# Kernel optimization log

Measured on AMD Instinct MI355X. Metric: run time of the kernel, lower is better.

## Reference

```python
import jax, jax.numpy as jnp
import numpy as np

B, C, H, W = 8, 512, 64, 64
CI = C // 8  # inter_channels = 64


def setup_inputs() -> dict:
    key = jax.random.key(0)
    k = jax.random.split(key, 8)
    s = 0.02
    return {
        "x": jax.random.normal(k[0], (B, C, H, W), dtype=jnp.float32),
        "wq": jax.random.normal(k[1], (CI, C), dtype=jnp.float32) * s,
        "bq": jnp.zeros((CI,), dtype=jnp.float32),
        "wk": jax.random.normal(k[2], (CI, C), dtype=jnp.float32) * s,
        "bk": jnp.zeros((CI,), dtype=jnp.float32),
        "wv": jax.random.normal(k[3], (C, C), dtype=jnp.float32) * s,
        "bv": jnp.zeros((C,), dtype=jnp.float32),
        # original inits gamma to 0 (which kills attention branch); use a
        # nonzero value so the attention path contributes to output/grads
        "gamma": jax.random.normal(k[4], (1,), dtype=jnp.float32),
    }


def reference(x, wq, bq, wk, bk, wv, bv, gamma):
    b, c, h, w = x.shape
    n = h * w
    xf = x.reshape(b, c, n)  # (B, C, HW)
    # 1x1 convs == per-pixel linear layers
    q = jnp.einsum("oc,bcn->bon", wq, xf) + bq[None, :, None]  # (B, CI, HW)
    k_ = jnp.einsum("oc,bcn->bon", wk, xf) + bk[None, :, None]  # (B, CI, HW)
    v = jnp.einsum("oc,bcn->bon", wv, xf) + bv[None, :, None]  # (B, C, HW)
    # energy[b, i, j] = <q[:, i], k[:, j]>  -> softmax over j
    energy = jnp.einsum("bdn,bdm->bnm", q, k_)  # (B, HW, HW)
    attn = jax.nn.softmax(energy, axis=-1)
    # note: torch code does bmm(value, attention) -> out[:, c, j] = sum_i v[:, c, i] * attn[:, i, j]
    out = jnp.einsum("bci,bij->bcj", v, attn).reshape(b, c, h, w)
    return gamma[0] * out + x
```

## Files before the change

### kernel.cpp

```cpp
#include <hip/hip_runtime.h>
#include <hip/hip_bf16.h>

#define N_TOK 4096
#define CCH   512

using f32x4  = __attribute__((ext_vector_type(4))) float;
using f32x16 = __attribute__((ext_vector_type(16))) float;
using bf16x4 = __attribute__((ext_vector_type(4))) short;
using bf16x8 = __attribute__((ext_vector_type(8))) short;
using u32x4  = __attribute__((ext_vector_type(4))) unsigned int;

__device__ __forceinline__ short f2bf(float f) {
  __hip_bfloat16 h = __float2bfloat16(f);
  return __builtin_bit_cast(short, h);
}

__device__ __forceinline__ unsigned pkexp(float a, float b) {
  unsigned ua = __builtin_bit_cast(unsigned, __expf(a));
  unsigned ub = __builtin_bit_cast(unsigned, __expf(b));
  ua = ua + 0x7fffu + ((ua >> 16) & 1u);
  ub = ub + 0x7fffu + ((ub >> 16) & 1u);
  return (ua >> 16) | (ub & 0xffff0000u);
}

__device__ __forceinline__ f32x4 mfma16(bf16x8 a, bf16x8 b, f32x4 c) {
  return __builtin_amdgcn_mfma_f32_16x16x32_bf16(a, b, c, 0, 0, 0);
}
__device__ __forceinline__ f32x16 mfma32(bf16x8 a, bf16x8 b, f32x16 c) {
  return __builtin_amdgcn_mfma_f32_32x32x16_bf16(a, b, c, 0, 0, 0);
}

__device__ __forceinline__ void gload16(const void* g, void* l) {
  __builtin_amdgcn_global_load_lds(
      (const __attribute__((address_space(1))) void*)g,
      (__attribute__((address_space(3))) void*)l, 16, 0, 0);
}

__device__ __forceinline__ void stage_tile(short* lds, const short* src, int src_stride,
                                           int granules, int tid, int nthr) {
  for (int g = tid; g < granules; g += nthr) {
    int r = g >> 3, c16 = g & 7;
    bf16x8 v = *(const bf16x8*)(src + r * src_stride + c16 * 8);
    *(bf16x8*)(lds + r * 64 + ((c16 ^ (r & 7)) * 8)) = v;
  }
}

__device__ __forceinline__ bf16x8 read_frag(const short* lds, int row0, int ks, int lane) {
  int r = row0 + (lane & 15);
  int c16 = ks * 4 + (lane >> 4);
  return *(const bf16x8*)(lds + r * 64 + ((c16 ^ (r & 7)) * 8));
}

__global__ void k_conv_w(const float* wq, const float* wk, const float* wv,
                         const float* bq, const float* bk,
                         short* wqk_bf, short* wv_bf, float* bqk) {
  int idx = blockIdx.x * blockDim.x + threadIdx.x;
  int stride = gridDim.x * blockDim.x;
  const int n1 = 128 * 512;
  const int n2 = 512 * 512;
  for (int i = idx; i < n1; i += stride) {
    int d = i >> 9, c = i & 511;
    float v = (d < 64) ? wq[d * 512 + c] : wk[(d - 64) * 512 + c];
    wqk_bf[i] = f2bf(v);
  }
  for (int i = idx; i < n2; i += stride) wv_bf[i] = f2bf(wv[i]);
  if (idx < 128) bqk[idx] = (idx < 64) ? bq[idx] : bk[idx - 64];
}

__global__ __launch_bounds__(256) void k_transpose_x(const float* x, short* xT) {
  __shared__ float tile[64][65];
  int b = blockIdx.z, c0 = blockIdx.y * 64, n0 = blockIdx.x * 64;
  int tid = threadIdx.x;
  int col = tid & 63, rowb = tid >> 6;
  for (int r = rowb; r < 64; r += 4)
    tile[r][col] = x[((long)b * CCH + c0 + r) * N_TOK + n0 + col];
  __syncthreads();
  for (int r = rowb; r < 64; r += 4)
    xT[((long)b * N_TOK + n0 + r) * CCH + c0 + col] = f2bf(tile[col][r]);
}

__global__ __launch_bounds__(256) void k_gemm_nt(
    const short* A, long long Ab, const short* Bt, long long Bb,
    short* out, long long Ob, int out_stride,
    const float* bias, int bias_row, const float* colscale, long long cs_stride, int K) {
  __shared__ short Al[128 * 64], Bl[128 * 64];
  int b = blockIdx.z;
  int m0 = blockIdx.y * 128, n0 = blockIdx.x * 128;
  int tid = threadIdx.x, lane = tid & 63, w = tid >> 6;
  int wm = w >> 1, wn = w & 1;
  const short* Ap = A + b * Ab + (long long)m0 * K;
  const short* Bp = Bt + b * Bb + (long long)n0 * K;
  f32x4 acc[4][4] = {};
  for (int kt = 0; kt < K; kt += 64) {
    __syncthreads();
    stage_tile(Al, Ap + kt, K, 1024, tid, 256);
    stage_tile(Bl, Bp + kt, K, 1024, tid, 256);
    __syncthreads();
    for (int ks = 0; ks < 2; ++ks) {
      bf16x8 af[4], bfr[4];
      for (int i = 0; i < 4; ++i) af[i] = read_frag(Al, wm * 64 + i * 16, ks, lane);
      for (int i = 0; i < 4; ++i) bfr[i] = read_frag(Bl, wn * 64 + i * 16, ks, lane);
      for (int mf = 0; mf < 4; ++mf)
        for (int nf = 0; nf < 4; ++nf)
          acc[mf][nf] = mfma16(af[mf], bfr[nf], acc[mf][nf]);
    }
  }
  for (int mf = 0; mf < 4; ++mf)
    for (int nf = 0; nf < 4; ++nf)
      for (int t = 0; t < 4; ++t) {
        int m = m0 + wm * 64 + mf * 16 + (lane >> 4) * 4 + t;
        int n = n0 + wn * 64 + nf * 16 + (lane & 15);
        float v = acc[mf][nf][t];
        v += bias_row ? bias[m] : bias[n];
        if (colscale) v *= colscale[b * cs_stride + n];
        out[b * Ob + (long long)m * out_stride + n] = f2bf(v);
      }
}

__global__ __launch_bounds__(256) void k_passA(const short* __restrict__ qkT,
                                               float* __restrict__ Zinv) {
  __shared__ short ql[128 * 64];
  __shared__ short kl[2][128 * 64];
  __shared__ float zbuf[4][128];
  const int b = blockIdx.y, i0 = blockIdx.x * 128;
  const int tid = threadIdx.x, lane = tid & 63, w = tid >> 6;
  const int l31 = lane & 31, hi = lane >> 5;
  const int x7 = l31 & 7;

  stage_tile(ql, qkT + ((long long)b * N_TOK + i0) * 128, 128, 1024, tid, 256);

  const short* ksrc[4];
#pragma unroll
  for (int q = 0; q < 4; ++q) {
    int idx = (w * 4 + q) * 64 + lane;
    int r = idx >> 3, g = idx & 7;
    ksrc[q] = qkT + ((long long)b * N_TOK + r) * 128 + 64 + ((g ^ (r & 7)) * 8);
  }
#define STAGEK(buf, jt)                                              \
  do {                                                               \
    _Pragma("unroll")                                                \
    for (int q = 0; q < 4; ++q)                                      \
      gload16(ksrc[q] + (long long)(jt) * 128 * 128,                 \
              &kl[buf][(w * 4 + q) * 512]);                          \
  } while (0)

  STAGEK(0, 0);
  __syncthreads();

  bf16x8 qfr[4][4];
#pragma unroll
  for (int f = 0; f < 4; ++f)
#pragma unroll
    for (int ks = 0; ks < 4; ++ks)
      qfr[f][ks] = *(const bf16x8*)(&ql[(f * 32 + l31) * 64 + (((2 * ks + hi) ^ x7) * 8)]);

  float zacc[4] = {0.f, 0.f, 0.f, 0.f};
#pragma unroll 1
  for (int jt = 0; jt < 32; ++jt) {
    const int cur = jt & 1;
    if (jt + 1 < 32) STAGEK(cur ^ 1, jt + 1);
    f32x16 sacc[4] = {};
#pragma unroll
    for (int ks = 0; ks < 4; ++ks) {
      bf16x8 kfr = *(const bf16x8*)(&kl[cur][(w * 32 + l31) * 64 + (((2 * ks + hi) ^ x7) * 8)]);
#pragma unroll
      for (int f = 0; f < 4; ++f) sacc[f] = mfma32(kfr, qfr[f][ks], sacc[f]);
    }
#pragma unroll
    for (int f = 0; f < 4; ++f)
#pragma unroll
      for (int t = 0; t < 16; ++t) zacc[f] += __expf(sacc[f][t]);
    __syncthreads();
  }
#undef STAGEK
#pragma unroll
  for (int f = 0; f < 4; ++f) {
    zacc[f] += __shfl_xor(zacc[f], 32, 64);
    if (hi == 0) zbuf[w][f * 32 + l31] = zacc[f];
  }
  __syncthreads();
  if (tid < 128) {
    float z = zbuf[0][tid] + zbuf[1][tid] + zbuf[2][tid] + zbuf[3][tid];
    Zinv[(long long)b * N_TOK + i0 + tid] = 1.0f / z;
  }
}

__global__ __launch_bounds__(512) void k_gemm_v(
    const short* __restrict__ wv_bf, const short* __restrict__ xT,
    const float* __restrict__ bv, const float* __restrict__ Zinv,
    short* __restrict__ v_bf) {
  __shared__ short Ab[2][256 * 64];
  __shared__ short Bb[2][256 * 64];
  const int b = blockIdx.z;
  const int n0 = blockIdx.x * 256, m0 = blockIdx.y * 256;
  const int tid = threadIdx.x;
  const int lane = tid & 63, w = tid >> 6;
  const int l31 = lane & 31, hi = lane >> 5;
  const int x7 = l31 & 7;
  const int mw = w >> 2, nw = w & 3;

  const short* asrc[4];
  const short* bsrc[4];
#pragma unroll
  for (int q = 0; q < 4; ++q) {
    int idx = (w * 4 + q) * 64 + lane;
    int r = idx >> 3, g = idx & 7;
    asrc[q] = wv_bf + (long long)(m0 + r) * 512 + ((g ^ (r & 7)) * 8);
    bsrc[q] = xT + ((long long)(b * N_TOK + n0 + r)) * 512 + ((g ^ (r & 7)) * 8);
  }
#define STAGEV(buf, kt)                                                   \
  do {                                                                    \
    _Pragma("unroll")                                                     \
    for (int q = 0; q < 4; ++q) {                                         \
      gload16(asrc[q] + (kt), &Ab[buf][(w * 4 + q) * 512]);               \
      gload16(bsrc[q] + (kt), &Bb[buf][(w * 4 + q) * 512]);               \
    }                                                                     \
  } while (0)

  f32x16 oacc[4][2] = {};
  STAGEV(0, 0);
#pragma unroll 1
  for (int t = 0; t < 8; ++t) {
    const int cur = t & 1;
    __syncthreads();
    if (t + 1 < 8) STAGEV(cur ^ 1, (t + 1) * 64);
#pragma unroll
    for (int ks = 0; ks < 4; ++ks) {
      const int gk = 2 * ks + hi;
      bf16x8 afr[4], bfr[2];
#pragma unroll
      for (int mf = 0; mf < 4; ++mf) {
        int row = mw * 128 + mf * 32 + l31;
        afr[mf] = *(const bf16x8*)(&Ab[cur][row * 64 + ((gk ^ x7) * 8)]);
      }
#pragma unroll
      for (int nf = 0; nf < 2; ++nf) {
        int row = nw * 64 + nf * 32 + l31;
        bfr[nf] = *(const bf16x8*)(&Bb[cur][row * 64 + ((gk ^ x7) * 8)]);
      }
#pragma unroll
      for (int mf = 0; mf < 4; ++mf)
#pragma unroll
        for (int nf = 0; nf < 2; ++nf)
          oacc[mf][nf] = mfma32(afr[mf], bfr[nf], oacc[mf][nf]);
    }
  }
#undef STAGEV

#pragma unroll
  for (int nf = 0; nf < 2; ++nf) {
    const int n = n0 + nw * 64 + nf * 32 + l31;
    const float zi = Zinv[(long long)b * N_TOK + n];
#pragma unroll
    for (int mf = 0; mf < 4; ++mf)
#pragma unroll
      for (int tt = 0; tt < 16; ++tt) {
        int m = m0 + mw * 128 + mf * 32 + ((tt & 3) + 8 * (tt >> 2) + 4 * hi);
        float v = (oacc[mf][nf][tt] + bv[m]) * zi;
        v_bf[((long long)(b * CCH + m)) * N_TOK + n] = f2bf(v);
      }
  }
}

__global__ __launch_bounds__(512, 2) void k_passB(
    const short* __restrict__ qkT, const short* __restrict__ v_bf,
    const float* __restrict__ x, const float* __restrict__ gamma_p,
    float* __restrict__ out) {
  __shared__ short ql[3][64 * 64];
  __shared__ short vl[3][256 * 64];
  const int b = blockIdx.z;
  const int j0 = blockIdx.x * 256;
  const int c0 = blockIdx.y * 256;
  const int tid = threadIdx.x;
  const int lane = tid & 63, w = tid >> 6;
  const int l31 = lane & 31, hi = lane >> 5;
  const int x7 = l31 & 7;
  const float gamma = *gamma_p;

  bf16x8 kf[4];
  {
    const short* kp = qkT + ((long long)b * N_TOK + j0 + w * 32 + l31) * 128 + 64 + hi * 8;
#pragma unroll
    for (int ks = 0; ks < 4; ++ks) kf[ks] = *(const bf16x8*)(kp + ks * 16);
  }

  const int qidx = w * 64 + lane;
  const int qr = qidx >> 3, qg = qidx & 7;
  const short* qsrc0 = qkT + ((long long)b * N_TOK + qr) * 128 + ((qg ^ (qr & 7)) * 8);
  const short* vsrc0[4];
#pragma unroll
  for (int q = 0; q < 4; ++q) {
    int idx = (w * 4 + q) * 64 + lane;
    int r = idx >> 3, g = idx & 7;
    vsrc0[q] = v_bf + ((long long)(b * CCH + c0 + r)) * N_TOK + ((g ^ (r & 7)) * 8);
  }

  f32x16 oacc[8] = {};

#define STAGE(buf, step)                                              \
  do {                                                                \
    gload16(qsrc0 + (long long)(step) * 64 * 128, &ql[buf][w * 512]); \
    _Pragma("unroll")                                                 \
    for (int q = 0; q < 4; ++q)                                       \
      gload16(vsrc0[q] + (step) * 64, &vl[buf][(w * 4 + q) * 512]);   \
  } while (0)

#define STEP(t, BUF)                                                          \
  do {                                                                        \
    if ((t) < 62) { asm volatile("s_waitcnt vmcnt(5)" ::: "memory"); }        \
    else          { asm volatile("s_waitcnt vmcnt(0)" ::: "memory"); }        \
    __builtin_amdgcn_s_barrier();                                             \
    asm volatile("" ::: "memory");                                            \
    __builtin_amdgcn_sched_barrier(0);                                        \
    if ((t) < 62) STAGE((BUF + 2) % 3, (t) + 2);                              \
    f32x16 sacc[2] = {};                                                      \
    _Pragma("unroll")                                                         \
    for (int ks = 0; ks < 4; ++ks) {                                          \
      int gq = ks * 2 + hi;                                                   \
      bf16x8 qf0 = *(const bf16x8*)(&ql[BUF][l31 * 64 + ((gq ^ x7) * 8)]);    \
      bf16x8 qf1 = *(const bf16x8*)(&ql[BUF][(32 + l31) * 64 + ((gq ^ x7) * 8)]); \
      sacc[0] = mfma32(qf0, kf[ks], sacc[0]);                                 \
      sacc[1] = mfma32(qf1, kf[ks], sacc[1]);                                 \
    }                                                                         \
    bf16x8 pb[4];                                                             \
    _Pragma("unroll")                                                         \
    for (int ks = 0; ks < 4; ++ks) {                                          \
      const int f = ks >> 1, kb = ks & 1;                                     \
      unsigned A0 = pkexp(sacc[f][8 * kb + 0], sacc[f][8 * kb + 1]);          \
      unsigned A1 = pkexp(sacc[f][8 * kb + 2], sacc[f][8 * kb + 3]);          \
      unsigned B0 = pkexp(sacc[f][8 * kb + 4], sacc[f][8 * kb + 5]);          \
      unsigned B1 = pkexp(sacc[f][8 * kb + 6], sacc[f][8 * kb + 7]);          \
      unsigned s0 = __shfl_xor(hi ? A0 : B0, 32, 64);                         \
      unsigned s1 = __shfl_xor(hi ? A1 : B1, 32, 64);                         \
      u32x4 wd = {hi ? s0 : A0, hi ? s1 : A1, hi ? B0 : s0, hi ? B1 : s1};    \
      pb[ks] = __builtin_bit_cast(bf16x8, wd);                                \
    }                                                                         \
    __builtin_amdgcn_s_setprio(1);                                            \
    _Pragma("unroll")                                                         \
    for (int ks = 0; ks < 4; ++ks) {                                          \
      const int gk = 2 * ks + hi;                                             \
      _Pragma("unroll")                                                       \
      for (int cf = 0; cf < 8; ++cf) {                                        \
        bf16x8 vf = *(const bf16x8*)(&vl[BUF][(cf * 32 + l31) * 64 + ((gk ^ x7) * 8)]); \
        oacc[cf] = mfma32(vf, pb[ks], oacc[cf]);                              \
      }                                                                       \
    }                                                                         \
    __builtin_amdgcn_s_setprio(0);                                            \
  } while (0)

  STAGE(0, 0);
  STAGE(1, 1);

#pragma unroll 1
  for (int t0 = 0; t0 < 63; t0 += 3) {
    STEP(t0 + 0, 0);
    STEP(t0 + 1, 1);
    STEP(t0 + 2, 2);
  }
  STEP(63, 0);
#undef STEP
#undef STAGE

  const float* xb = x + (long long)b * CCH * N_TOK;
  float* ob = out + (long long)b * CCH * N_TOK;
  const int j = j0 + w * 32 + l31;
#pragma unroll
  for (int cf = 0; cf < 8; ++cf)
#pragma unroll
    for (int tt = 0; tt < 16; ++tt) {
      int c = c0 + cf * 32 + ((tt & 3) + 8 * (tt >> 2) + 4 * hi);
      long long idx = (long long)c * N_TOK + j;
      ob[idx] = gamma * oacc[cf][tt] + xb[idx];
    }
}

extern "C" void kernel_launch(void* const* d_in, const int* in_sizes, int n_in,
                              void* d_out, int out_size, void* d_ws, size_t ws_size,
                              hipStream_t stream) {
  const float* x     = (const float*)d_in[0];
  const float* wq    = (const float*)d_in[1];
  const float* bq    = (const float*)d_in[2];
  const float* wk    = (const float*)d_in[3];
  const float* bk    = (const float*)d_in[4];
  const float* wv    = (const float*)d_in[5];
  const float* bv    = (const float*)d_in[6];
  const float* gamma = (const float*)d_in[7];
  float* out = (float*)d_out;
  char* ws = (char*)d_ws;

  short* xT     = (short*)(ws);
  short* qkT    = (short*)(ws + 33554432);
  short* v_bf   = (short*)(ws + 41943040);
  float* Zinv   = (float*)(ws + 75497472);
  short* wqk_bf = (short*)(ws + 75628544);
  short* wv_bf  = (short*)(ws + 75759616);
  float* bqk    = (float*)(ws + 76283904);

  k_conv_w<<<dim3(256), dim3(256), 0, stream>>>(wq, wk, wv, bq, bk, wqk_bf, wv_bf, bqk);
  k_transpose_x<<<dim3(64, 8, 8), dim3(256), 0, stream>>>(x, xT);
  k_gemm_nt<<<dim3(1, 32, 8), dim3(256), 0, stream>>>(
      xT, (long long)4096 * 512, wqk_bf, (long long)0,
      qkT, (long long)4096 * 128, 128, bqk, 0, nullptr, 0, 512);
  k_passA<<<dim3(32, 8), dim3(256), 0, stream>>>(qkT, Zinv);
  k_gemm_v<<<dim3(16, 2, 8), dim3(512), 0, stream>>>(wv_bf, xT, bv, Zinv, v_bf);
  k_passB<<<dim3(16, 2, 8), dim3(512), 0, stream>>>(qkT, v_bf, x, gamma, out);
}
```

Baseline: 306.2 us.

## Replace generic QK GEMM with double-buffered 32x32 MFMA kernel, vectorize transpose

The generic NT GEMM for the Q/K projection is replaced by a dedicated kernel. It uses 512 threads, 32x32x16 MFMAs and double-buffered LDS tiles filled by asynchronous global-to-LDS loads, so the next K tile loads while the current one computes. The x transpose now reads float4 and writes bf16x4 vectors instead of scalar elements. The new GEMM has hardcoded shapes, and its output stores are strided two-byte writes to qkT.

```diff
diff --git a/kernel.cpp b/kernel.cpp
--- a/kernel.cpp
+++ b/kernel.cpp
@@ -23,9 +23,6 @@
   return (ua >> 16) | (ub & 0xffff0000u);
 }
 
-__device__ __forceinline__ f32x4 mfma16(bf16x8 a, bf16x8 b, f32x4 c) {
-  return __builtin_amdgcn_mfma_f32_16x16x32_bf16(a, b, c, 0, 0, 0);
-}
 __device__ __forceinline__ f32x16 mfma32(bf16x8 a, bf16x8 b, f32x16 c) {
   return __builtin_amdgcn_mfma_f32_32x32x16_bf16(a, b, c, 0, 0, 0);
 }
@@ -43,12 +40,6 @@
     bf16x8 v = *(const bf16x8*)(src + r * src_stride + c16 * 8);
     *(bf16x8*)(lds + r * 64 + ((c16 ^ (r & 7)) * 8)) = v;
   }
-}
-
-__device__ __forceinline__ bf16x8 read_frag(const short* lds, int row0, int ks, int lane) {
-  int r = row0 + (lane & 15);
-  int c16 = ks * 4 + (lane >> 4);
-  return *(const bf16x8*)(lds + r * 64 + ((c16 ^ (r & 7)) * 8));
 }
 
 __global__ void k_conv_w(const float* wq, const float* wk, const float* wv,
@@ -67,54 +58,91 @@
   if (idx < 128) bqk[idx] = (idx < 64) ? bq[idx] : bk[idx - 64];
 }
 
-__global__ __launch_bounds__(256) void k_transpose_x(const float* x, short* xT) {
+__global__ __launch_bounds__(256) void k_transpose_x(const float* __restrict__ x,
+                                                     short* __restrict__ xT) {
   __shared__ float tile[64][65];
-  int b = blockIdx.z, c0 = blockIdx.y * 64, n0 = blockIdx.x * 64;
-  int tid = threadIdx.x;
-  int col = tid & 63, rowb = tid >> 6;
-  for (int r = rowb; r < 64; r += 4)
-    tile[r][col] = x[((long)b * CCH + c0 + r) * N_TOK + n0 + col];
+  const int b = blockIdx.z, c0 = blockIdx.y * 64, n0 = blockIdx.x * 64;
+  const int tid = threadIdx.x;
+  const int q = tid & 15, r0 = tid >> 4;
+#pragma unroll
+  for (int p = 0; p < 4; ++p) {
+    int c = r0 + p * 16;
+    f32x4 v = *(const f32x4*)&x[((long)b * CCH + c0 + c) * N_TOK + n0 + q * 4];
+    tile[c][q * 4 + 0] = v[0]; tile[c][q * 4 + 1] = v[1];
+    tile[c][q * 4 + 2] = v[2]; tile[c][q * 4 + 3] = v[3];
+  }
   __syncthreads();
-  for (int r = rowb; r < 64; r += 4)
-    xT[((long)b * N_TOK + n0 + r) * CCH + c0 + col] = f2bf(tile[col][r]);
-}
-
-__global__ __launch_bounds__(256) void k_gemm_nt(
-    const short* A, long long Ab, const short* Bt, long long Bb,
-    short* out, long long Ob, int out_stride,
-    const float* bias, int bias_row, const float* colscale, long long cs_stride, int K) {
-  __shared__ short Al[128 * 64], Bl[128 * 64];
-  int b = blockIdx.z;
-  int m0 = blockIdx.y * 128, n0 = blockIdx.x * 128;
-  int tid = threadIdx.x, lane = tid & 63, w = tid >> 6;
-  int wm = w >> 1, wn = w & 1;
-  const short* Ap = A + b * Ab + (long long)m0 * K;
-  const short* Bp = Bt + b * Bb + (long long)n0 * K;
-  f32x4 acc[4][4] = {};
-  for (int kt = 0; kt < K; kt += 64) {
+#pragma unroll
+  for (int p = 0; p < 4; ++p) {
+    int n = r0 + p * 16;
+    bf16x4 o;
+    o[0] = f2bf(tile[q * 4 + 0][n]); o[1] = f2bf(tile[q * 4 + 1][n]);
+    o[2] = f2bf(tile[q * 4 + 2][n]); o[3] = f2bf(tile[q * 4 + 3][n]);
+    *(bf16x4*)&xT[((long)b * N_TOK + n0 + n) * CCH + c0 + q * 4] = o;
+  }
+}
+
+__global__ __launch_bounds__(512) void k_gemm_qk(
+    const short* __restrict__ xT, const short* __restrict__ wqk_bf,
+    const float* __restrict__ bqk, short* __restrict__ qkT) {
+  __shared__ short An[2][128 * 64];
+  __shared__ short Bm[2][128 * 64];
+  const int b = blockIdx.z;
+  const int n0 = blockIdx.x * 128;
+  const int tid = threadIdx.x, lane = tid & 63, w = tid >> 6;
+  const int l31 = lane & 31, hi = lane >> 5, x7 = l31 & 7;
+  const int nw = w & 3, mw = w >> 2;
+
+  const short* asrc[2];
+  const short* bsrc[2];
+#pragma unroll
+  for (int q = 0; q < 2; ++q) {
+    int idx = (w * 2 + q) * 64 + lane;
+    int r = idx >> 3, g = idx & 7;
+    asrc[q] = xT + ((long long)(b * N_TOK + n0 + r)) * 512 + ((g ^ (r & 7)) * 8);
+    bsrc[q] = wqk_bf + (long long)r * 512 + ((g ^ (r & 7)) * 8);
+  }
+#define STAGEQK(buf, kt)                                           \
+  do {                                                             \
+    _Pragma("unroll")                                              \
+    for (int q = 0; q < 2; ++q) {                                  \
+      gload16(asrc[q] + (kt), &An[buf][(w * 2 + q) * 512]);        \
+      gload16(bsrc[q] + (kt), &Bm[buf][(w * 2 + q) * 512]);        \
+    }                                                              \
+  } while (0)
+
+  f32x16 oacc[2] = {};
+  STAGEQK(0, 0);
+#pragma unroll 1
+  for (int t = 0; t < 8; ++t) {
+    const int cur = t & 1;
     __syncthreads();
-    stage_tile(Al, Ap + kt, K, 1024, tid, 256);
-    stage_tile(Bl, Bp + kt, K, 1024, tid, 256);
-    __syncthreads();
-    for (int ks = 0; ks < 2; ++ks) {
-      bf16x8 af[4], bfr[4];
-      for (int i = 0; i < 4; ++i) af[i] = read_frag(Al, wm * 64 + i * 16, ks, lane);
-      for (int i = 0; i < 4; ++i) bfr[i] = read_frag(Bl, wn * 64 + i * 16, ks, lane);
-      for (int mf = 0; mf < 4; ++mf)
-        for (int nf = 0; nf < 4; ++nf)
-          acc[mf][nf] = mfma16(af[mf], bfr[nf], acc[mf][nf]);
+    if (t + 1 < 8) STAGEQK(cur ^ 1, (t + 1) * 64);
+#pragma unroll
+    for (int ks = 0; ks < 4; ++ks) {
+      const int gk = 2 * ks + hi;
+      int nrow = nw * 32 + l31;
+      bf16x8 anf = *(const bf16x8*)(&An[cur][nrow * 64 + ((gk ^ x7) * 8)]);
+#pragma unroll
+      for (int mf = 0; mf < 2; ++mf) {
+        int mrow = mw * 64 + mf * 32 + l31;
+        bf16x8 bmf = *(const bf16x8*)(&Bm[cur][mrow * 64 + ((gk ^ x7) * 8)]);
+        oacc[mf] = mfma32(anf, bmf, oacc[mf]);
+      }
     }
   }
-  for (int mf = 0; mf < 4; ++mf)
-    for (int nf = 0; nf < 4; ++nf)
-      for (int t = 0; t < 4; ++t) {
-        int m = m0 + wm * 64 + mf * 16 + (lane >> 4) * 4 + t;
-        int n = n0 + wn * 64 + nf * 16 + (lane & 15);
-        float v = acc[mf][nf][t];
-        v += bias_row ? bias[m] : bias[n];
-        if (colscale) v *= colscale[b * cs_stride + n];
-        out[b * Ob + (long long)m * out_stride + n] = f2bf(v);
-      }
+#undef STAGEQK
+
+#pragma unroll
+  for (int mf = 0; mf < 2; ++mf) {
+    const int m = mw * 64 + mf * 32 + l31;
+    const float bias = bqk[m];
+#pragma unroll
+    for (int tt = 0; tt < 16; ++tt) {
+      int n = n0 + nw * 32 + ((tt & 3) + 8 * (tt >> 2) + 4 * hi);
+      qkT[((long long)(b * N_TOK + n)) * 128 + m] = f2bf(oacc[mf][tt] + bias);
+    }
+  }
 }
 
 __global__ __launch_bounds__(256) void k_passA(const short* __restrict__ qkT,
@@ -398,9 +426,7 @@
 
   k_conv_w<<<dim3(256), dim3(256), 0, stream>>>(wq, wk, wv, bq, bk, wqk_bf, wv_bf, bqk);
   k_transpose_x<<<dim3(64, 8, 8), dim3(256), 0, stream>>>(x, xT);
-  k_gemm_nt<<<dim3(1, 32, 8), dim3(256), 0, stream>>>(
-      xT, (long long)4096 * 512, wqk_bf, (long long)0,
-      qkT, (long long)4096 * 128, 128, bqk, 0, nullptr, 0, 512);
+  k_gemm_qk<<<dim3(32, 1, 8), dim3(512), 0, stream>>>(xT, wqk_bf, bqk, qkT);
   k_passA<<<dim3(32, 8), dim3(256), 0, stream>>>(qkT, Zinv);
   k_gemm_v<<<dim3(16, 2, 8), dim3(512), 0, stream>>>(wv_bf, xT, bv, Zinv, v_bf);
   k_passB<<<dim3(16, 2, 8), dim3(512), 0, stream>>>(qkT, v_bf, x, gamma, out);
```

New measurement: 285.0 us. -6.9%, faster.
